# Kernel tuning notes

Hardware: AMD Instinct MI355X
Metric: run time of the kernel (lower is better)

Reference implementation:

```python
import jax, jax.numpy as jnp
import numpy as np

N, CS, CZ, H, C, PQ, PV, N0, N1 = 768, 384, 128, 12, 64, 4, 8, 192, 64
CZ4 = CZ // 4
INF, EPS = 1e5, 1e-8


def setup_inputs() -> dict:
    key = jax.random.key(0)
    ks = jax.random.split(key, 24)

    def w(k, i, o):
        return jax.random.normal(k, (i, o), jnp.float32) / np.float32(np.sqrt(i))

    s = jax.random.normal(ks[0], (N, CS), jnp.float32)
    z = jax.random.normal(ks[1], (N, N, CZ), jnp.float32)
    rot = jnp.linalg.qr(jax.random.normal(ks[2], (N, 3, 3), jnp.float32))[0]
    trans = jax.random.normal(ks[3], (N, 3), jnp.float32)
    mask = jnp.ones((N,), jnp.float32)
    is_atom = jax.random.bernoulli(ks[4], 0.5, (N,))
    return dict(
        s=s, z=z, rot=rot, trans=trans, mask=mask, is_atom=is_atom,
        wq=w(ks[5], CS, H * C), bq=jnp.zeros((H * C,), jnp.float32),
        wkv=w(ks[6], CS, 2 * H * C), bkv=jnp.zeros((2 * H * C,), jnp.float32),
        wqp=w(ks[7], CS, 3 * H * PQ), bqp=jnp.zeros((3 * H * PQ,), jnp.float32),
        wkvp=w(ks[8], CS, 3 * H * (PQ + PV)), bkvp=jnp.zeros((3 * H * (PQ + PV),), jnp.float32),
        wb=w(ks[9], CZ, H), bb=jnp.zeros((H,), jnp.float32),
        wdz=w(ks[10], CZ, CZ4), bdz=jnp.zeros((CZ4,), jnp.float32),
        head_weights=jnp.full((H,), 0.5413248, jnp.float32),  # softplus^-1(1), per ipa_point_weights_init_
        wout=w(ks[11], H * (C + 4 * PV + CZ4), CS), bout=jnp.zeros((CS,), jnp.float32),
        tfnq_ws=w(ks[12], N0, H * C), tfnq_wv=w(ks[13], N1, H * PQ),
        tfnkv_ws=w(ks[14], N0, 2 * H * C), tfnkv_wv=w(ks[15], N1, H * (PQ + PV)),
        tfno_ws=w(ks[16], H * (C + PV + CZ4), N0), tfno_wv=w(ks[17], H * PV, N1),
    )


def reference(s, z, rot, trans, mask, is_atom, wq, bq, wkv, bkv, wqp, bqp, wkvp, bkvp,
              wb, bb, wdz, bdz, head_weights, wout, bout,
              tfnq_ws, tfnq_wv, tfnkv_ws, tfnkv_wv, tfno_ws, tfno_wv):
    n = s.shape[0]

    def apply_rigid(pts):  # pts: [n, P, 3] -> R x + t
        return jnp.einsum('nij,npj->npi', rot, pts) + trans[:, None, :]

    # ---- residue (frame) path ----
    q_r = (s @ wq + bq).reshape(n, H, C)
    kv_r = (s @ wkv + bkv).reshape(n, H, 2 * C)
    k_r, v_r = kv_r[..., :C], kv_r[..., C:]
    # torch.split-in-3 then stack(dim=-1) layout: [n, 3, H*P] -> [n, H*P, 3]
    qp = (s @ wqp + bqp).reshape(n, 3, H * PQ).transpose(0, 2, 1)
    q_pts_r = apply_rigid(qp).reshape(n, H, PQ, 3)
    kvp = (s @ wkvp + bkvp).reshape(n, 3, H * (PQ + PV)).transpose(0, 2, 1)
    kv_pts_r = apply_rigid(kvp).reshape(n, H, PQ + PV, 3)
    k_pts_r, v_pts_r = kv_pts_r[..., :PQ, :], kv_pts_r[..., PQ:, :]

    # ---- atom (TFN-equivariant) path: irreps = N0 scalars + N1 vectors ----
    sc = s[:, :N0]
    vec = s[:, N0:N0 + 3 * N1].reshape(n, N1, 3)
    q_a = (sc @ tfnq_ws).reshape(n, H, C)
    q_pts_a = jnp.einsum('nix,io->nox', vec, tfnq_wv).reshape(n, H, PQ, 3) + trans[:, None, None, :]
    kv_a = (sc @ tfnkv_ws).reshape(n, H, 2 * C)
    k_a, v_a = kv_a[..., :C], kv_a[..., C:]
    kv_pts_a = jnp.einsum('nix,io->nox', vec, tfnkv_wv).reshape(n, H, PQ + PV, 3) + trans[:, None, None, :]
    k_pts_a, v_pts_a = kv_pts_a[..., :PQ, :], kv_pts_a[..., PQ:, :]

    m1 = is_atom[:, None, None]
    m2 = is_atom[:, None, None, None]
    q = jnp.where(m1, q_a, q_r)
    k = jnp.where(m1, k_a, k_r)
    v = jnp.where(m1, v_a, v_r)
    q_pts = jnp.where(m2, q_pts_a, q_pts_r)
    k_pts = jnp.where(m2, k_pts_a, k_pts_r)
    v_pts = jnp.where(m2, v_pts_a, v_pts_r)

    # ---- attention logits ----
    b = z @ wb + bb  # [n, n, H]
    a = jnp.einsum('nhc,mhc->hnm', q, k) * np.float32(np.sqrt(1.0 / (3 * C)))
    a = a + np.float32(np.sqrt(1.0 / 3)) * b.transpose(2, 0, 1)

    disp = q_pts[:, None] - k_pts[None]          # [n, n, H, PQ, 3]
    pt_att = jnp.sum(disp * disp, axis=-1)       # [n, n, H, PQ]
    hw = jax.nn.softplus(head_weights) * np.float32(np.sqrt(1.0 / (3 * (PQ * 9.0 / 2))))
    pt_att = -0.5 * jnp.sum(pt_att * hw[:, None], axis=-1)  # [n, n, H]
    a = a + pt_att.transpose(2, 0, 1)

    sq_mask = INF * (mask[:, None] * mask[None, :] - 1.0)
    a = jax.nn.softmax(a + sq_mask[None], axis=-1)  # [H, n, n]

    # ---- aggregation ----
    o = jnp.einsum('hnm,mhc->nhc', a, v).reshape(n, H * C)
    o_pt = jnp.einsum('hnm,mhpx->nhpx', a, v_pts)  # [n, H, PV, 3]
    o_pt = jnp.einsum('nji,nhpj->nhpi', rot, o_pt - trans[:, None, None, :])  # invert_apply
    o_pt_norm = jnp.sqrt(jnp.sum(o_pt * o_pt, axis=-1) + EPS).reshape(n, H * PV)
    o_pt = o_pt.reshape(n, H * PV, 3)
    pair_z = z @ wdz + bdz  # [n, n, CZ4]
    o_pair = jnp.einsum('hnm,nmz->nhz', a, pair_z).reshape(n, H * CZ4)

    # ---- residue output head ----
    res_feats = jnp.concatenate([o, o_pt[..., 0], o_pt[..., 1], o_pt[..., 2], o_pt_norm, o_pair], axis=-1)
    res_out = res_feats @ wout + bout  # [n, CS]

    # ---- atom output head (equivariant linear: scalars mix, vectors mix per-component) ----
    atom_sc = jnp.concatenate([o, o_pt_norm, o_pair], axis=-1) @ tfno_ws  # [n, N0]
    atom_vec = jnp.einsum('npx,po->nox', o_pt, tfno_wv).reshape(n, 3 * N1)
    atom_out = jnp.concatenate([atom_sc, atom_vec], axis=-1)  # [n, CS]

    return jnp.where(is_atom[:, None], atom_out, res_out)
```

## Files before the change

### kernel.cpp

```cpp
#include <hip/hip_runtime.h>
#include <hip/hip_bf16.h>

static constexpr int NN = 768;

typedef short v8bf __attribute__((ext_vector_type(8)));
typedef float v4f  __attribute__((ext_vector_type(4)));

__device__ __forceinline__ unsigned short f2bf(float f) {
  unsigned u = __float_as_uint(f);
  u += 0x7fffu + ((u >> 16) & 1u);
  return (unsigned short)(u >> 16);
}
__device__ __forceinline__ float bf2f(unsigned short s) {
  return __uint_as_float(((unsigned)s) << 16);
}

static constexpr size_t OFF_ISA    = 0;
static constexpr size_t OFF_WCT    = 1024;
static constexpr size_t OFF_BCAT   = 4096;
static constexpr size_t OFF_SBF    = 4160;
static constexpr size_t OFF_WQT    = 151616;
static constexpr size_t OFF_WKVT   = 299072;
static constexpr size_t OFF_WQPT   = 593984;
static constexpr size_t OFF_WKVPT  = 630848;
static constexpr size_t OFF_TFNQT  = 716864;
static constexpr size_t OFF_TFNKVT = 815168;
static constexpr size_t OFF_WOUTT  = 1011776;
static constexpr size_t OFF_TFNOT  = 1306688;
static constexpr size_t OFF_QR     = 1429568;
static constexpr size_t OFF_KVR    = 1724480;
static constexpr size_t OFF_QP     = 2314304;
static constexpr size_t OFF_KVP    = 2424896;
static constexpr size_t OFF_QA     = 2756672;
static constexpr size_t OFF_KVA    = 3051584;
static constexpr size_t OFF_QCAT   = 3641408;
static constexpr size_t OFF_KCAT   = 4083776;
static constexpr size_t OFF_RQ     = 4526144;
static constexpr size_t OFF_RK     = 4535360;
static constexpr size_t OFF_VCATT  = 4986944;
static constexpr size_t OFF_BB     = 5429312;
static constexpr size_t OFF_PZT    = 8968256;
static constexpr size_t OFF_ABF    = 18405440;
static constexpr size_t OFF_OPTRAW = 21944384;
static constexpr size_t OFF_RESF   = 22165568;
static constexpr size_t OFF_ATOMF  = 22755392;

__device__ void transpose_cv(const float* __restrict__ src, unsigned short* __restrict__ dst,
                             int K, int Kp, int N, int ky, int nx) {
  __shared__ float tl[32][33];
  const int k0 = ky * 32, n0 = nx * 32;
  const int tx = threadIdx.x & 31, ty = threadIdx.x >> 5;
  for (int it = 0; it < 4; ++it) {
    int r = ty + it * 8;
    float v = 0.f;
    if (k0 + r < K && n0 + tx < N) v = src[(long long)(k0 + r) * N + n0 + tx];
    tl[r][tx] = v;
  }
  __syncthreads();
  for (int it = 0; it < 4; ++it) {
    int r = ty + it * 8;
    if (n0 + r < N && k0 + tx < Kp)
      dst[(long long)(n0 + r) * Kp + k0 + tx] = f2bf(tl[tx][r]);
  }
}

__global__ __launch_bounds__(256) void prep0(
    float* wsf, const float* s, const float* wq, const float* wkv,
    const float* wqp, const float* wkvp, const float* tfnq_ws,
    const float* tfnkv_ws, const float* wout, const float* tfno_ws,
    const float* wb, const float* wdz, const float* bb, const float* bdz,
    const unsigned int* isa_raw)
{
  const int bx = blockIdx.x, t = threadIdx.x;
  if (bx < 288)       { int g = bx;        transpose_cv(wq,      (unsigned short*)(wsf+OFF_WQT),    384, 384, 768,  g/24, g%24); return; }
  else if (bx < 864)  { int g = bx-288;    transpose_cv(wkv,     (unsigned short*)(wsf+OFF_WKVT),   384, 384, 1536, g/48, g%48); return; }
  else if (bx < 924)  { int g = bx-864;    transpose_cv(wqp,     (unsigned short*)(wsf+OFF_WQPT),   384, 384, 144,  g/5,  g%5);  return; }
  else if (bx < 1092) { int g = bx-924;    transpose_cv(wkvp,    (unsigned short*)(wsf+OFF_WKVPT),  384, 384, 432,  g/14, g%14); return; }
  else if (bx < 1284) { int g = bx-1092;   transpose_cv(tfnq_ws, (unsigned short*)(wsf+OFF_TFNQT),  192, 256, 768,  g/24, g%24); return; }
  else if (bx < 1668) { int g = bx-1284;   transpose_cv(tfnkv_ws,(unsigned short*)(wsf+OFF_TFNKVT), 192, 256, 1536, g/48, g%48); return; }
  else if (bx < 2244) { int g = bx-1668;   transpose_cv(wout,    (unsigned short*)(wsf+OFF_WOUTT),  1536,1536,384,  g/12, g%12); return; }
  else if (bx < 2484) { int g = bx-2244;   transpose_cv(tfno_ws, (unsigned short*)(wsf+OFF_TFNOT),  1248,1280,192,  g/6,  g%6);  return; }
  else if (bx < 2772) {
    long long base = (long long)(bx - 2484) * 1024 + t * 4;
    float4 v = *(const float4*)(s + base);
    unsigned short tmp[4] = {f2bf(v.x), f2bf(v.y), f2bf(v.z), f2bf(v.w)};
    *(uint2*)((unsigned short*)(wsf + OFF_SBF) + base) = *(uint2*)tmp;
    return;
  } else if (bx < 2773) {
    __shared__ int notint, notfloat;
    int* ISA = (int*)(wsf + OFF_ISA);
    if (t == 0) { notint = 0; notfloat = 0; }
    __syncthreads();
    if (t < 192) {
      unsigned v = isa_raw[t];
      if (v > 1u) atomicOr(&notint, 1);
      if (v != 0u && v != 0x3F800000u) atomicOr(&notfloat, 1);
    }
    __syncthreads();
    const int mode = (!notint) ? 0 : ((!notfloat) ? 1 : 2);
    for (int n = t; n < NN; n += 256) {
      int val;
      if (mode == 2) val = (((const unsigned char*)isa_raw)[n] != 0);
      else           val = (isa_raw[n] != 0u);
      ISA[n] = val;
    }
    return;
  } else {
    const float rs3 = 0.57735026918962576f;
    unsigned short* WCT = (unsigned short*)(wsf + OFF_WCT);
    float* bcat = wsf + OFF_BCAT;
    int idx = (bx - 2773) * 256 + t;
    if (idx < 48 * 128) {
      int o = idx >> 7, k = idx & 127;
      float v = 0.f;
      if (o < 12) v = rs3 * wb[k * 12 + o];
      else if (o < 44) v = wdz[k * 32 + (o - 12)];
      WCT[o * 128 + k] = f2bf(v);
    }
    if (bx == 2773 && t < 48)
      bcat[t] = (t < 12) ? rs3 * bb[t] : (t < 44 ? bdz[t - 12] : 0.f);
  }
}

__device__ __forceinline__ void gemm16(
    char* lds, const unsigned short* __restrict__ A, int lda,
    const unsigned short* __restrict__ BT, int ldb, int KQ,
    const float* __restrict__ bias, int mode,
    float* Cf, unsigned short* Cb, int ldc, int Nc, int colb, int row0,
    const int* __restrict__ ISA, float* outp)
{
  v4f (*PS)[4][64] = (v4f (*)[4][64])lds;
  const int t = threadIdx.x, w = t >> 6, l = t & 63, l15 = l & 15, lg = l >> 4;
  const int rowA = row0 + l15;
  v4f acc[4] = {};
  const unsigned short* ap = A + (long long)rowA * lda + lg * 8;
  const int kend = (w + 1) * KQ;
  for (int k0 = w * KQ; k0 < kend; k0 += 32) {
    v8bf av = *(const v8bf*)(ap + k0);
#pragma unroll
    for (int cf = 0; cf < 4; ++cf) {
      v8bf bv = *(const v8bf*)(BT + (long long)(colb + cf * 16 + l15) * ldb + k0 + lg * 8);
      acc[cf] = __builtin_amdgcn_mfma_f32_16x16x32_bf16(av, bv, acc[cf], 0, 0, 0);
    }
  }
#pragma unroll
  for (int cf = 0; cf < 4; ++cf) PS[w][cf][l] = acc[cf];
  __syncthreads();
  const int cf = w;
  v4f sv = PS[0][cf][l] + PS[1][cf][l] + PS[2][cf][l] + PS[3][cf][l];
  const int c = colb + cf * 16 + l15;
  if (c < Nc) {
    float bvs = bias ? bias[c] : 0.f;
#pragma unroll
    for (int i = 0; i < 4; ++i) {
      int r = row0 + lg * 4 + i;
      float v = sv[i] + bvs;
      if (mode == 0)      Cf[(long long)r * ldc + c] = v;
      else if (mode == 1) Cb[(long long)r * ldc + c] = f2bf(v);
      else if (mode == 2) { if (!ISA[r]) outp[r * 384 + c] = v; }
      else                { if ( ISA[r]) outp[r * 384 + c] = v; }
    }
  }
}

__global__ __launch_bounds__(256) void mega1(
    float* wsf, const float* __restrict__ z,
    const float* bq, const float* bkv, const float* bqp, const float* bkvp)
{
  __shared__ __align__(16) char lds[23296];
  const int t = threadIdx.x;
  if (blockIdx.x < 4608) {
    float* Sout = (float*)lds;
    const unsigned short* WCT = (const unsigned short*)(wsf + OFF_WCT);
    const float* bcat = wsf + OFF_BCAT;
    unsigned short* Bb  = (unsigned short*)(wsf + OFF_BB);
    unsigned short* PZT = (unsigned short*)(wsf + OFF_PZT);
    const long long row0 = (long long)blockIdx.x * 128;
    const int w = t >> 6, l = t & 63, l15 = l & 15, lg = l >> 4;
    v8bf bvv[4][3];
#pragma unroll
    for (int ks = 0; ks < 4; ++ks)
#pragma unroll
      for (int cf = 0; cf < 3; ++cf)
        bvv[ks][cf] = *(const v8bf*)(WCT + (cf * 16 + l15) * 128 + ks * 32 + lg * 8);
    v4f acc[2][3] = {};
#pragma unroll
    for (int rf = 0; rf < 2; ++rf) {
      const float* zrow = z + (row0 + w * 32 + rf * 16 + l15) * 128 + lg * 8;
#pragma unroll
      for (int ks = 0; ks < 4; ++ks) {
        float4 a0 = *(const float4*)(zrow + ks * 32);
        float4 a1 = *(const float4*)(zrow + ks * 32 + 4);
        unsigned short tmp[8] = {f2bf(a0.x), f2bf(a0.y), f2bf(a0.z), f2bf(a0.w),
                                 f2bf(a1.x), f2bf(a1.y), f2bf(a1.z), f2bf(a1.w)};
        v8bf av = *(const v8bf*)tmp;
#pragma unroll
        for (int cf = 0; cf < 3; ++cf)
          acc[rf][cf] = __builtin_amdgcn_mfma_f32_16x16x32_bf16(av, bvv[ks][cf], acc[rf][cf], 0, 0, 0);
      }
    }
#pragma unroll
    for (int rf = 0; rf < 2; ++rf)
#pragma unroll
      for (int cf = 0; cf < 3; ++cf) {
        int o = cf * 16 + l15;
#pragma unroll
        for (int i = 0; i < 4; ++i) {
          int m = w * 32 + rf * 16 + lg * 4 + i;
          Sout[o * 132 + m] = acc[rf][cf][i];
        }
      }
    __syncthreads();
    const int n = blockIdx.x / 6;
    const int m0 = (blockIdx.x % 6) * 128;
    for (int idx = t; idx < 44 * 8; idx += 256) {
      int o = idx >> 3, seg = idx & 7;
      float bias = bcat[o];
      unsigned short tmp[16];
#pragma unroll
      for (int j = 0; j < 16; ++j) tmp[j] = f2bf(Sout[o * 132 + seg * 16 + j] + bias);
      unsigned short* gp;
      if (o < 12) gp = Bb + ((long long)o * 768 + n) * 768 + m0 + seg * 16;
      else        gp = PZT + ((long long)n * 32 + (o - 12)) * 768 + m0 + seg * 16;
      *(uint4*)gp = *(uint4*)tmp;
      *(uint4*)(gp + 8) = *(uint4*)(tmp + 8);
    }
    return;
  }
  const int g = blockIdx.x - 4608;
  const int bt = g / 82, xt = g % 82;
  const unsigned short* SBF = (const unsigned short*)(wsf + OFF_SBF);
  const unsigned short* BT; const float* bias; int ldb, KQ, mode, ldc, Nc, colb;
  float* Cf = nullptr; unsigned short* Cb = nullptr;
  if (xt < 12)      { BT=(const unsigned short*)(wsf+OFF_WQT);    bias=bq;     ldb=384; KQ=96; Cb=(unsigned short*)(wsf+OFF_QR);  ldc=768;  Nc=768;  colb=xt*64;      mode=1; }
  else if (xt < 36) { BT=(const unsigned short*)(wsf+OFF_WKVT);   bias=bkv;    ldb=384; KQ=96; Cb=(unsigned short*)(wsf+OFF_KVR); ldc=1536; Nc=1536; colb=(xt-12)*64; mode=1; }
  else if (xt < 39) { BT=(const unsigned short*)(wsf+OFF_WQPT);   bias=bqp;    ldb=384; KQ=96; Cf=wsf+OFF_QP;                     ldc=144;  Nc=144;  colb=(xt-36)*64; mode=0; }
  else if (xt < 46) { BT=(const unsigned short*)(wsf+OFF_WKVPT);  bias=bkvp;   ldb=384; KQ=96; Cf=wsf+OFF_KVP;                    ldc=432;  Nc=432;  colb=(xt-39)*64; mode=0; }
  else if (xt < 58) { BT=(const unsigned short*)(wsf+OFF_TFNQT);  bias=nullptr;ldb=256; KQ=64; Cb=(unsigned short*)(wsf+OFF_QA);  ldc=768;  Nc=768;  colb=(xt-46)*64; mode=1; }
  else              { BT=(const unsigned short*)(wsf+OFF_TFNKVT); bias=nullptr;ldb=256; KQ=64; Cb=(unsigned short*)(wsf+OFF_KVA); ldc=1536; Nc=1536; colb=(xt-58)*64; mode=1; }
  gemm16(lds, SBF, 384, BT, ldb, KQ, bias, mode, Cf, Cb, ldc, Nc, colb, bt * 16, nullptr, nullptr);
}

__global__ __launch_bounds__(256) void prep_qkv(
    float* wsf, const float* __restrict__ s,
    const float* __restrict__ rot, const float* __restrict__ trans,
    const float* __restrict__ head_w,
    const float* __restrict__ tfnq_wv, const float* __restrict__ tfnkv_wv)
{
  const int n = blockIdx.x, t = threadIdx.x;
  const int* ISA = (const int*)(wsf + OFF_ISA);
  const unsigned short* QRb  = (const unsigned short*)(wsf + OFF_QR);
  const unsigned short* KVRb = (const unsigned short*)(wsf + OFF_KVR);
  const unsigned short* QAb  = (const unsigned short*)(wsf + OFF_QA);
  const unsigned short* KVAb = (const unsigned short*)(wsf + OFF_KVA);
  const float* QP  = wsf + OFF_QP;
  const float* KVP = wsf + OFF_KVP;
  unsigned short* Qcat = (unsigned short*)(wsf + OFF_QCAT);
  unsigned short* Kcat = (unsigned short*)(wsf + OFF_KCAT);
  unsigned short* Vt   = (unsigned short*)(wsf + OFF_VCATT);
  float* rq = wsf + OFF_RQ;
  float* rk = wsf + OFF_RK;
  const bool isa = ISA[n] != 0;
  __shared__ float R[9], T[3], shw[12], sv[192];
  __shared__ float qs[768], ks[768], vs[768], qp[144], kp[144], vp[288];
  if (t < 9) R[t] = rot[n * 9 + t];
  if (t < 3) T[t] = trans[n * 3 + t];
  if (t >= 16 && t < 28)
    shw[t - 16] = log1pf(__expf(head_w[t - 16])) * 0.13608276348795434f;
  if (isa && t >= 32 && t < 224) sv[t - 32] = s[(size_t)n * 384 + 192 + (t - 32)];
  __syncthreads();
  for (int idx = t; idx < 768; idx += 256) {
    int h = idx >> 6, c = idx & 63;
    qs[idx] = bf2f(isa ? QAb[(long long)n * 768 + idx] : QRb[(long long)n * 768 + idx]);
    ks[idx] = bf2f(isa ? KVAb[(long long)n * 1536 + h * 128 + c] : KVRb[(long long)n * 1536 + h * 128 + c]);
    vs[idx] = bf2f(isa ? KVAb[(long long)n * 1536 + h * 128 + 64 + c] : KVRb[(long long)n * 1536 + h * 128 + 64 + c]);
  }
  if (isa) {
    for (int idx = t; idx < 144; idx += 256) {
      int hp = idx / 3, x = idx % 3;
      float a = 0.f;
      for (int i = 0; i < 64; ++i) a += sv[i * 3 + x] * tfnq_wv[i * 48 + hp];
      qp[idx] = a + T[x];
    }
    for (int idx = t; idx < 432; idx += 256) {
      int o = idx / 3, x = idx % 3;
      float a = 0.f;
      for (int i = 0; i < 64; ++i) a += sv[i * 3 + x] * tfnkv_wv[i * 144 + o];
      float v = a + T[x];
      int h = o / 12, pp = o % 12;
      if (pp < 4) kp[(h * 4 + pp) * 3 + x] = v;
      else        vp[(h * 8 + (pp - 4)) * 3 + x] = v;
    }
  } else {
    for (int idx = t; idx < 144; idx += 256) {
      int hp = idx / 3, i = idx % 3;
      qp[idx] = R[i * 3 + 0] * QP[(long long)n * 144 + 0 + hp] +
                R[i * 3 + 1] * QP[(long long)n * 144 + 48 + hp] +
                R[i * 3 + 2] * QP[(long long)n * 144 + 96 + hp] + T[i];
    }
    for (int idx = t; idx < 432; idx += 256) {
      int hp = idx / 3, i = idx % 3;
      float v = R[i * 3 + 0] * KVP[(long long)n * 432 + 0 + hp] +
                R[i * 3 + 1] * KVP[(long long)n * 432 + 144 + hp] +
                R[i * 3 + 2] * KVP[(long long)n * 432 + 288 + hp] + T[i];
      int h = hp / 12, pp = hp % 12;
      if (pp < 4) kp[(h * 4 + pp) * 3 + i] = v;
      else        vp[(h * 8 + (pp - 4)) * 3 + i] = v;
    }
  }
  __syncthreads();
  const float sq = 0.07216878364870322f;
  for (int idx = t; idx < 1152; idx += 256) {
    int h = idx / 96, c = idx % 96;
    float qv = (c < 64) ? sq * qs[h * 64 + c] : ((c < 76) ? shw[h] * qp[h * 12 + (c - 64)] : 0.f);
    float kv = (c < 64) ? ks[h * 64 + c]      : ((c < 76) ? kp[h * 12 + (c - 64)] : 0.f);
    float vv = (c < 64) ? vs[h * 64 + c]      : ((c < 88) ? vp[h * 24 + (c - 64)] : 0.f);
    long long base = ((long long)n * 12 + h) * 96 + c;
    Qcat[base] = f2bf(qv);
    Kcat[base] = f2bf(kv);
    Vt[((long long)h * 96 + c) * 768 + n] = f2bf(vv);
  }
  if (t < 24) {
    int h = t >> 1, which = t & 1;
    const float* p = which ? kp : qp;
    float s2 = 0.f;
#pragma unroll
    for (int d = 0; d < 12; ++d) { float x = p[h * 12 + d]; s2 += x * x; }
    float val = 0.5f * shw[h] * s2;
    if (which) rk[h * 768 + n] = val;
    else       rq[h * 768 + n] = val;
  }
}

__global__ __launch_bounds__(256) void mega2(float* wsf, const float* __restrict__ mask) {
  __shared__ __align__(16) char lds[26112];
  const int t = threadIdx.x;
  const unsigned short* Qcat = (const unsigned short*)(wsf + OFF_QCAT);
  const unsigned short* Kcat = (const unsigned short*)(wsf + OFF_KCAT);
  const unsigned short* Bb   = (const unsigned short*)(wsf + OFF_BB);
  const unsigned short* VcatT= (const unsigned short*)(wsf + OFF_VCATT);
  const float* rq = wsf + OFF_RQ;
  const float* rk = wsf + OFF_RK;
  unsigned short* Abf   = (unsigned short*)(wsf + OFF_ABF);
  unsigned short* RESF  = (unsigned short*)(wsf + OFF_RESF);
  unsigned short* ATOMF = (unsigned short*)(wsf + OFF_ATOMF);
  float* OPTRAW = wsf + OFF_OPTRAW;
  const int h = blockIdx.x / 48, r0 = (blockIdx.x % 48) * 16;
  const int w = t >> 6, l = t & 63, l15 = l & 15, lg = l >> 4;
  unsigned short* SW = (unsigned short*)lds + w * 3200;
  float* redm = (float*)(lds + 25600);
  float* reds = (float*)(lds + 25856);
  const int nrow = r0 + l15;
  v8bf aq[3];
#pragma unroll
  for (int ks = 0; ks < 3; ++ks)
    aq[ks] = *(const v8bf*)(Qcat + ((long long)nrow * 12 + h) * 96 + ks * 32 + lg * 8);
  v4f acc[12] = {};
#pragma unroll
  for (int cf = 0; cf < 12; ++cf) {
    int m = w * 192 + cf * 16 + l15;
    const unsigned short* kb = Kcat + ((long long)m * 12 + h) * 96 + lg * 8;
#pragma unroll
    for (int ks = 0; ks < 3; ++ks) {
      v8bf bv = *(const v8bf*)(kb + ks * 32);
      acc[cf] = __builtin_amdgcn_mfma_f32_16x16x32_bf16(aq[ks], bv, acc[cf], 0, 0, 0);
    }
  }
#pragma unroll
  for (int it = 0; it < 6; ++it) {
    int chunk = it * 64 + l;
    int row = chunk / 24, cc = (chunk % 24) * 8;
    *(uint4*)(SW + row * 200 + cc) =
        *(const uint4*)(Bb + ((long long)(h * 768 + r0 + row)) * 768 + w * 192 + cc);
  }
  __syncthreads();
  float rkm[12], mkm[12];
#pragma unroll
  for (int cf = 0; cf < 12; ++cf) {
    int m = w * 192 + cf * 16 + l15;
    rkm[cf] = rk[h * 768 + m];
    mkm[cf] = mask[m];
  }
  float rqn[4], mkn[4], mymax[4];
#pragma unroll
  for (int i = 0; i < 4; ++i) {
    int gn = r0 + lg * 4 + i;
    rqn[i] = rq[h * 768 + gn];
    mkn[i] = mask[gn];
    mymax[i] = -3.0e38f;
  }
#pragma unroll
  for (int cf = 0; cf < 12; ++cf)
#pragma unroll
    for (int i = 0; i < 4; ++i) {
      float v = acc[cf][i] + bf2f(SW[(lg * 4 + i) * 200 + cf * 16 + l15])
              - rqn[i] - rkm[cf] + 100000.0f * (mkn[i] * mkm[cf] - 1.0f);
      acc[cf][i] = v;
      mymax[i] = fmaxf(mymax[i], v);
    }
#pragma unroll
  for (int off = 1; off < 16; off <<= 1)
#pragma unroll
    for (int i = 0; i < 4; ++i) mymax[i] = fmaxf(mymax[i], __shfl_xor(mymax[i], off, 64));
  if (l15 == 0) {
#pragma unroll
    for (int i = 0; i < 4; ++i) redm[w * 16 + lg * 4 + i] = mymax[i];
  }
  __syncthreads();
  float mx[4], mysum[4];
#pragma unroll
  for (int i = 0; i < 4; ++i) {
    int rl = lg * 4 + i;
    mx[i] = fmaxf(fmaxf(redm[rl], redm[16 + rl]), fmaxf(redm[32 + rl], redm[48 + rl]));
    mysum[i] = 0.f;
  }
#pragma unroll
  for (int cf = 0; cf < 12; ++cf)
#pragma unroll
    for (int i = 0; i < 4; ++i) {
      float e = __expf(acc[cf][i] - mx[i]);
      acc[cf][i] = e;
      mysum[i] += e;
    }
#pragma unroll
  for (int off = 1; off < 16; off <<= 1)
#pragma unroll
    for (int i = 0; i < 4; ++i) mysum[i] += __shfl_xor(mysum[i], off, 64);
  if (l15 == 0) {
#pragma unroll
    for (int i = 0; i < 4; ++i) reds[w * 16 + lg * 4 + i] = mysum[i];
  }
  __syncthreads();
  float inv[4];
#pragma unroll
  for (int i = 0; i < 4; ++i) {
    int rl = lg * 4 + i;
    inv[i] = 1.0f / (reds[rl] + reds[16 + rl] + reds[32 + rl] + reds[48 + rl]);
  }
#pragma unroll
  for (int cf = 0; cf < 12; ++cf)
#pragma unroll
    for (int i = 0; i < 4; ++i)
      SW[(lg * 4 + i) * 200 + cf * 16 + l15] = f2bf(acc[cf][i] * inv[i]);
  __syncthreads();
#pragma unroll
  for (int it = 0; it < 6; ++it) {
    int chunk = it * 64 + l;
    int row = chunk / 24, cc = (chunk % 24) * 8;
    *(uint4*)(Abf + ((long long)(h * 768 + r0 + row)) * 768 + w * 192 + cc) =
        *(const uint4*)(SW + row * 200 + cc);
  }
  const unsigned short* vbase = VcatT + (long long)h * 96 * 768 + w * 192 + lg * 8;
  v4f acc2[6] = {};
  for (int kk = 0; kk < 192; kk += 32) {
    v8bf av = *(const v8bf*)(SW + l15 * 200 + kk + lg * 8);
#pragma unroll
    for (int cf = 0; cf < 6; ++cf) {
      v8bf bv = *(const v8bf*)(vbase + (long long)(cf * 16 + l15) * 768 + kk);
      acc2[cf] = __builtin_amdgcn_mfma_f32_16x16x32_bf16(av, bv, acc2[cf], 0, 0, 0);
    }
  }
  __syncthreads();
  v4f (*PS)[64] = (v4f (*)[64])lds;
#pragma unroll
  for (int cf = 0; cf < 6; ++cf) PS[w * 6 + cf][l] = acc2[cf];
  __syncthreads();
  for (int cf = w; cf < 6; cf += 4) {
    v4f sv = PS[cf][l] + PS[6 + cf][l] + PS[12 + cf][l] + PS[18 + cf][l];
    int c = cf * 16 + l15;
    int rb = r0 + lg * 4;
#pragma unroll
    for (int i = 0; i < 4; ++i) {
      int n = rb + i;
      float v = sv[i];
      if (c < 64) {
        unsigned short b = f2bf(v);
        RESF[(long long)n * 1536 + h * 64 + c] = b;
        ATOMF[(long long)n * 1280 + h * 64 + c] = b;
      } else if (c < 88) {
        OPTRAW[(long long)n * 288 + h * 24 + (c - 64)] = v;
      }
    }
  }
}

__global__ __launch_bounds__(256) void mega3(
    float* wsf, const float* __restrict__ rot, const float* __restrict__ trans,
    const float* __restrict__ tfno_wv, float* __restrict__ out)
{
  const int t = threadIdx.x;
  unsigned short* RESF  = (unsigned short*)(wsf + OFF_RESF);
  unsigned short* ATOMF = (unsigned short*)(wsf + OFF_ATOMF);
  if (blockIdx.x < 768) {
    __shared__ __align__(16) v4f PS[8][64];
    const unsigned short* Abf = (const unsigned short*)(wsf + OFF_ABF);
    const unsigned short* PZT = (const unsigned short*)(wsf + OFF_PZT);
    const int w = t >> 6, l = t & 63, l15 = l & 15, lg = l >> 4;
    const int n = blockIdx.x;
    const int hh = (l15 < 12) ? l15 : 0;
    const unsigned short* arow = Abf + ((long long)hh * 768 + n) * 768 + lg * 8;
    const unsigned short* pz = PZT + (long long)n * 32 * 768 + lg * 8;
    v4f acc[2] = {};
    for (int k0 = w * 192; k0 < w * 192 + 192; k0 += 32) {
      v8bf av = *(const v8bf*)(arow + k0);
#pragma unroll
      for (int cf = 0; cf < 2; ++cf) {
        v8bf bv = *(const v8bf*)(pz + (long long)(cf * 16 + l15) * 768 + k0);
        acc[cf] = __builtin_amdgcn_mfma_f32_16x16x32_bf16(av, bv, acc[cf], 0, 0, 0);
      }
    }
    PS[w * 2 + 0][l] = acc[0];
    PS[w * 2 + 1][l] = acc[1];
    __syncthreads();
    if (t < 128) {
      int cf = t >> 6, ll = t & 63;
      v4f sv = PS[cf][ll] + PS[2 + cf][ll] + PS[4 + cf][ll] + PS[6 + cf][ll];
      int zc = cf * 16 + (ll & 15);
#pragma unroll
      for (int i = 0; i < 4; ++i) {
        int hd = (ll >> 4) * 4 + i;
        if (hd < 12) {
          unsigned short b = f2bf(sv[i]);
          RESF[(long long)n * 1536 + 1152 + hd * 32 + zc] = b;
          ATOMF[(long long)n * 1280 + 864 + hd * 32 + zc] = b;
        }
      }
    }
    return;
  }
  {
    const int n = blockIdx.x - 768;
    const float* OPTRAW = wsf + OFF_OPTRAW;
    const int* ISA = (const int*)(wsf + OFF_ISA);
    const bool isa = ISA[n] != 0;
    __shared__ float R[9], T[3], opt2[96][3], norml[96];
    if (t < 9) R[t] = rot[(size_t)n * 9 + t];
    if (t < 3) T[t] = trans[(size_t)n * 3 + t];
    __syncthreads();
    for (int idx = t; idx < 288; idx += 256) {
      int hp = idx / 3, i = idx % 3;
      float x = OPTRAW[(size_t)n * 288 + hp * 3 + 0] - T[0];
      float y = OPTRAW[(size_t)n * 288 + hp * 3 + 1] - T[1];
      float z = OPTRAW[(size_t)n * 288 + hp * 3 + 2] - T[2];
      opt2[hp][i] = R[0 + i] * x + R[3 + i] * y + R[6 + i] * z;
    }
    __syncthreads();
    if (t < 96)
      norml[t] = sqrtf(opt2[t][0] * opt2[t][0] + opt2[t][1] * opt2[t][1] +
                       opt2[t][2] * opt2[t][2] + 1e-8f);
    __syncthreads();
    const long long rb = (long long)n * 1536;
    const long long ab = (long long)n * 1280;
    for (int idx = t; idx < 288; idx += 256) {
      int x = idx / 96, hp = idx % 96;
      RESF[rb + 768 + idx] = f2bf(opt2[hp][x]);
    }
    for (int idx = t; idx < 96; idx += 256) {
      unsigned short b = f2bf(norml[idx]);
      RESF[rb + 1056 + idx] = b;
      ATOMF[ab + 768 + idx] = b;
    }
    if (isa) {
      for (int idx = t; idx < 192; idx += 256) {
        int o = idx / 3, x = idx % 3;
        float a = 0.f;
        for (int p = 0; p < 96; ++p) a += opt2[p][x] * tfno_wv[p * 64 + o];
        out[(size_t)n * 384 + 192 + idx] = a;
      }
    }
  }
}

__global__ __launch_bounds__(256) void outg(float* wsf, const float* __restrict__ bout,
                                            float* __restrict__ out) {
  __shared__ __align__(16) char lds[16384];
  const int g = blockIdx.x;
  const int bt = g / 9, xt = g % 9;
  const int* ISA = (const int*)(wsf + OFF_ISA);
  if (xt < 6)
    gemm16(lds, (const unsigned short*)(wsf + OFF_RESF), 1536,
           (const unsigned short*)(wsf + OFF_WOUTT), 1536, 384, bout, 2,
           nullptr, nullptr, 0, 384, xt * 64, bt * 16, ISA, out);
  else
    gemm16(lds, (const unsigned short*)(wsf + OFF_ATOMF), 1280,
           (const unsigned short*)(wsf + OFF_TFNOT), 1280, 320, nullptr, 3,
           nullptr, nullptr, 0, 192, (xt - 6) * 64, bt * 16, ISA, out);
}

extern "C" void kernel_launch(void* const* d_in, const int* in_sizes, int n_in,
                              void* d_out, int out_size, void* d_ws, size_t ws_size,
                              hipStream_t stream) {
  (void)in_sizes; (void)n_in; (void)out_size; (void)ws_size;
  const float* s      = (const float*)d_in[0];
  const float* z      = (const float*)d_in[1];
  const float* rot    = (const float*)d_in[2];
  const float* trans  = (const float*)d_in[3];
  const float* mask   = (const float*)d_in[4];
  const float* wq     = (const float*)d_in[6];
  const float* bq     = (const float*)d_in[7];
  const float* wkv    = (const float*)d_in[8];
  const float* bkv    = (const float*)d_in[9];
  const float* wqp    = (const float*)d_in[10];
  const float* bqp    = (const float*)d_in[11];
  const float* wkvp   = (const float*)d_in[12];
  const float* bkvp   = (const float*)d_in[13];
  const float* wb     = (const float*)d_in[14];
  const float* bb     = (const float*)d_in[15];
  const float* wdz    = (const float*)d_in[16];
  const float* bdz    = (const float*)d_in[17];
  const float* head_w = (const float*)d_in[18];
  const float* wout   = (const float*)d_in[19];
  const float* bout   = (const float*)d_in[20];
  const float* tfnq_ws  = (const float*)d_in[21];
  const float* tfnq_wv  = (const float*)d_in[22];
  const float* tfnkv_ws = (const float*)d_in[23];
  const float* tfnkv_wv = (const float*)d_in[24];
  const float* tfno_ws  = (const float*)d_in[25];
  const float* tfno_wv  = (const float*)d_in[26];

  float* wsf = (float*)d_ws;

  prep0<<<2797, 256, 0, stream>>>(wsf, s, wq, wkv, wqp, wkvp, tfnq_ws, tfnkv_ws,
                                  wout, tfno_ws, wb, wdz, bb, bdz,
                                  (const unsigned int*)d_in[5]);
  mega1<<<8544, 256, 0, stream>>>(wsf, z, bq, bkv, bqp, bkvp);
  prep_qkv<<<768, 256, 0, stream>>>(wsf, s, rot, trans, head_w, tfnq_wv, tfnkv_wv);
  mega2<<<576, 256, 0, stream>>>(wsf, mask);
  mega3<<<1536, 256, 0, stream>>>(wsf, rot, trans, tfno_wv, (float*)d_out);
  outg<<<432, 256, 0, stream>>>(wsf, bout, (float*)d_out);
}
```

Before: 186.1 us.

## Split z-projection pass across two kernels to overlap with weight prep and GEMMs

The large z projection pass (4608 blocks) moves out of a single kernel and is split into two halves. The first half runs alongside the weight transposes and the s conversion, and the second half runs alongside the projection GEMMs. The small WCT/bias/is_atom setup moves into a tiny leading kernel because the z pass depends on it. The goal is to hide the prep work and the GEMM tail behind the memory-bound z streaming, at the cost of one extra kernel launch; an unroll pragma is also added in mega2.

After: 200.2 us. +7.6%, slower.

```diff
diff --git a/kernel.cpp b/kernel.cpp
--- a/kernel.cpp
+++ b/kernel.cpp
@@ -45,9 +45,50 @@
 static constexpr size_t OFF_RESF   = 22165568;
 static constexpr size_t OFF_ATOMF  = 22755392;
 
-__device__ void transpose_cv(const float* __restrict__ src, unsigned short* __restrict__ dst,
+__global__ __launch_bounds__(256) void tiny0(
+    float* wsf, const float* __restrict__ wb, const float* __restrict__ wdz,
+    const float* __restrict__ bb, const float* __restrict__ bdz,
+    const unsigned int* __restrict__ isa_raw)
+{
+  const int t = threadIdx.x;
+  if (blockIdx.x == 0) {
+    const float rs3 = 0.57735026918962576f;
+    unsigned short* WCT = (unsigned short*)(wsf + OFF_WCT);
+    float* bcat = wsf + OFF_BCAT;
+    for (int idx = t; idx < 48 * 128; idx += 256) {
+      int o = idx >> 7, k = idx & 127;
+      float v = 0.f;
+      if (o < 12) v = rs3 * wb[k * 12 + o];
+      else if (o < 44) v = wdz[k * 32 + (o - 12)];
+      WCT[o * 128 + k] = f2bf(v);
+    }
+    if (t < 48)
+      bcat[t] = (t < 12) ? rs3 * bb[t] : (t < 44 ? bdz[t - 12] : 0.f);
+  } else {
+    __shared__ int notint, notfloat;
+    int* ISA = (int*)wsf;
+    if (t == 0) { notint = 0; notfloat = 0; }
+    __syncthreads();
+    if (t < 192) {
+      unsigned v = isa_raw[t];
+      if (v > 1u) atomicOr(&notint, 1);
+      if (v != 0u && v != 0x3F800000u) atomicOr(&notfloat, 1);
+    }
+    __syncthreads();
+    const int mode = (!notint) ? 0 : ((!notfloat) ? 1 : 2);
+    for (int n = t; n < NN; n += 256) {
+      int val;
+      if (mode == 2) val = (((const unsigned char*)isa_raw)[n] != 0);
+      else           val = (isa_raw[n] != 0u);
+      ISA[n] = val;
+    }
+  }
+}
+
+__device__ void transpose_cv(char* ldsbuf, const float* __restrict__ src,
+                             unsigned short* __restrict__ dst,
                              int K, int Kp, int N, int ky, int nx) {
-  __shared__ float tl[32][33];
+  float (*tl)[33] = (float (*)[33])ldsbuf;
   const int k0 = ky * 32, n0 = nx * 32;
   const int tx = threadIdx.x & 31, ty = threadIdx.x >> 5;
   for (int it = 0; it < 4; ++it) {
@@ -61,64 +102,6 @@
     int r = ty + it * 8;
     if (n0 + r < N && k0 + tx < Kp)
       dst[(long long)(n0 + r) * Kp + k0 + tx] = f2bf(tl[tx][r]);
-  }
-}
-
-__global__ __launch_bounds__(256) void prep0(
-    float* wsf, const float* s, const float* wq, const float* wkv,
-    const float* wqp, const float* wkvp, const float* tfnq_ws,
-    const float* tfnkv_ws, const float* wout, const float* tfno_ws,
-    const float* wb, const float* wdz, const float* bb, const float* bdz,
-    const unsigned int* isa_raw)
-{
-  const int bx = blockIdx.x, t = threadIdx.x;
-  if (bx < 288)       { int g = bx;        transpose_cv(wq,      (unsigned short*)(wsf+OFF_WQT),    384, 384, 768,  g/24, g%24); return; }
-  else if (bx < 864)  { int g = bx-288;    transpose_cv(wkv,     (unsigned short*)(wsf+OFF_WKVT),   384, 384, 1536, g/48, g%48); return; }
-  else if (bx < 924)  { int g = bx-864;    transpose_cv(wqp,     (unsigned short*)(wsf+OFF_WQPT),   384, 384, 144,  g/5,  g%5);  return; }
-  else if (bx < 1092) { int g = bx-924;    transpose_cv(wkvp,    (unsigned short*)(wsf+OFF_WKVPT),  384, 384, 432,  g/14, g%14); return; }
-  else if (bx < 1284) { int g = bx-1092;   transpose_cv(tfnq_ws, (unsigned short*)(wsf+OFF_TFNQT),  192, 256, 768,  g/24, g%24); return; }
-  else if (bx < 1668) { int g = bx-1284;   transpose_cv(tfnkv_ws,(unsigned short*)(wsf+OFF_TFNKVT), 192, 256, 1536, g/48, g%48); return; }
-  else if (bx < 2244) { int g = bx-1668;   transpose_cv(wout,    (unsigned short*)(wsf+OFF_WOUTT),  1536,1536,384,  g/12, g%12); return; }
-  else if (bx < 2484) { int g = bx-2244;   transpose_cv(tfno_ws, (unsigned short*)(wsf+OFF_TFNOT),  1248,1280,192,  g/6,  g%6);  return; }
-  else if (bx < 2772) {
-    long long base = (long long)(bx - 2484) * 1024 + t * 4;
-    float4 v = *(const float4*)(s + base);
-    unsigned short tmp[4] = {f2bf(v.x), f2bf(v.y), f2bf(v.z), f2bf(v.w)};
-    *(uint2*)((unsigned short*)(wsf + OFF_SBF) + base) = *(uint2*)tmp;
-    return;
-  } else if (bx < 2773) {
-    __shared__ int notint, notfloat;
-    int* ISA = (int*)(wsf + OFF_ISA);
-    if (t == 0) { notint = 0; notfloat = 0; }
-    __syncthreads();
-    if (t < 192) {
-      unsigned v = isa_raw[t];
-      if (v > 1u) atomicOr(&notint, 1);
-      if (v != 0u && v != 0x3F800000u) atomicOr(&notfloat, 1);
-    }
-    __syncthreads();
-    const int mode = (!notint) ? 0 : ((!notfloat) ? 1 : 2);
-    for (int n = t; n < NN; n += 256) {
-      int val;
-      if (mode == 2) val = (((const unsigned char*)isa_raw)[n] != 0);
-      else           val = (isa_raw[n] != 0u);
-      ISA[n] = val;
-    }
-    return;
-  } else {
-    const float rs3 = 0.57735026918962576f;
-    unsigned short* WCT = (unsigned short*)(wsf + OFF_WCT);
-    float* bcat = wsf + OFF_BCAT;
-    int idx = (bx - 2773) * 256 + t;
-    if (idx < 48 * 128) {
-      int o = idx >> 7, k = idx & 127;
-      float v = 0.f;
-      if (o < 12) v = rs3 * wb[k * 12 + o];
-      else if (o < 44) v = wdz[k * 32 + (o - 12)];
-      WCT[o * 128 + k] = f2bf(v);
-    }
-    if (bx == 2773 && t < 48)
-      bcat[t] = (t < 12) ? rs3 * bb[t] : (t < 44 ? bdz[t - 12] : 0.f);
   }
 }
 
@@ -163,71 +146,96 @@
   }
 }
 
-__global__ __launch_bounds__(256) void mega1(
+__device__ void zpass_body(char* lds, float* wsf, const float* __restrict__ z, int bx) {
+  const int t = threadIdx.x;
+  float* Sout = (float*)lds;
+  const unsigned short* WCT = (const unsigned short*)(wsf + OFF_WCT);
+  const float* bcat = wsf + OFF_BCAT;
+  unsigned short* Bb  = (unsigned short*)(wsf + OFF_BB);
+  unsigned short* PZT = (unsigned short*)(wsf + OFF_PZT);
+  const long long row0 = (long long)bx * 128;
+  const int w = t >> 6, l = t & 63, l15 = l & 15, lg = l >> 4;
+  v8bf bvv[4][3];
+#pragma unroll
+  for (int ks = 0; ks < 4; ++ks)
+#pragma unroll
+    for (int cf = 0; cf < 3; ++cf)
+      bvv[ks][cf] = *(const v8bf*)(WCT + (cf * 16 + l15) * 128 + ks * 32 + lg * 8);
+  v4f acc[2][3] = {};
+#pragma unroll
+  for (int rf = 0; rf < 2; ++rf) {
+    const float* zrow = z + (row0 + w * 32 + rf * 16 + l15) * 128 + lg * 8;
+#pragma unroll
+    for (int ks = 0; ks < 4; ++ks) {
+      float4 a0 = *(const float4*)(zrow + ks * 32);
+      float4 a1 = *(const float4*)(zrow + ks * 32 + 4);
+      unsigned short tmp[8] = {f2bf(a0.x), f2bf(a0.y), f2bf(a0.z), f2bf(a0.w),
+                               f2bf(a1.x), f2bf(a1.y), f2bf(a1.z), f2bf(a1.w)};
+      v8bf av = *(const v8bf*)tmp;
+#pragma unroll
+      for (int cf = 0; cf < 3; ++cf)
+        acc[rf][cf] = __builtin_amdgcn_mfma_f32_16x16x32_bf16(av, bvv[ks][cf], acc[rf][cf], 0, 0, 0);
+    }
+  }
+#pragma unroll
+  for (int rf = 0; rf < 2; ++rf)
+#pragma unroll
+    for (int cf = 0; cf < 3; ++cf) {
+      int o = cf * 16 + l15;
+#pragma unroll
+      for (int i = 0; i < 4; ++i) {
+        int m = w * 32 + rf * 16 + lg * 4 + i;
+        Sout[o * 132 + m] = acc[rf][cf][i];
+      }
+    }
+  __syncthreads();
+  const int n = bx / 6;
+  const int m0 = (bx % 6) * 128;
+  for (int idx = t; idx < 44 * 8; idx += 256) {
+    int o = idx >> 3, seg = idx & 7;
+    float bias = bcat[o];
+    unsigned short tmp[16];
+#pragma unroll
+    for (int j = 0; j < 16; ++j) tmp[j] = f2bf(Sout[o * 132 + seg * 16 + j] + bias);
+    unsigned short* gp;
+    if (o < 12) gp = Bb + ((long long)o * 768 + n) * 768 + m0 + seg * 16;
+    else        gp = PZT + ((long long)n * 32 + (o - 12)) * 768 + m0 + seg * 16;
+    *(uint4*)gp = *(uint4*)tmp;
+    *(uint4*)(gp + 8) = *(uint4*)(tmp + 8);
+  }
+}
+
+__global__ __launch_bounds__(256) void zmix1(
+    float* wsf, const float* __restrict__ z, const float* s,
+    const float* wq, const float* wkv, const float* wqp, const float* wkvp,
+    const float* tfnq_ws, const float* tfnkv_ws, const float* wout, const float* tfno_ws)
+{
+  __shared__ __align__(16) char lds[23296];
+  if (blockIdx.x < 2304) { zpass_body(lds, wsf, z, blockIdx.x); return; }
+  const int vb = blockIdx.x - 2304;
+  if (vb < 288)       { transpose_cv(lds, wq,       (unsigned short*)(wsf+OFF_WQT),    384, 384, 768,  vb/24,        vb%24); }
+  else if (vb < 864)  { int g = vb-288;  transpose_cv(lds, wkv,      (unsigned short*)(wsf+OFF_WKVT),   384, 384, 1536, g/48, g%48); }
+  else if (vb < 924)  { int g = vb-864;  transpose_cv(lds, wqp,      (unsigned short*)(wsf+OFF_WQPT),   384, 384, 144,  g/5,  g%5);  }
+  else if (vb < 1092) { int g = vb-924;  transpose_cv(lds, wkvp,     (unsigned short*)(wsf+OFF_WKVPT),  384, 384, 432,  g/14, g%14); }
+  else if (vb < 1284) { int g = vb-1092; transpose_cv(lds, tfnq_ws,  (unsigned short*)(wsf+OFF_TFNQT),  192, 256, 768,  g/24, g%24); }
+  else if (vb < 1668) { int g = vb-1284; transpose_cv(lds, tfnkv_ws, (unsigned short*)(wsf+OFF_TFNKVT), 192, 256, 1536, g/48, g%48); }
+  else if (vb < 2244) { int g = vb-1668; transpose_cv(lds, wout,     (unsigned short*)(wsf+OFF_WOUTT),  1536,1536,384,  g/12, g%12); }
+  else if (vb < 2484) { int g = vb-2244; transpose_cv(lds, tfno_ws,  (unsigned short*)(wsf+OFF_TFNOT),  1248,1280,192,  g/6,  g%6);  }
+  else {
+    long long base = (long long)(vb - 2484) * 1024 + threadIdx.x * 4;
+    float4 v = *(const float4*)(s + base);
+    unsigned short tmp[4] = {f2bf(v.x), f2bf(v.y), f2bf(v.z), f2bf(v.w)};
+    *(uint2*)((unsigned short*)(wsf + OFF_SBF) + base) = *(uint2*)tmp;
+  }
+}
+
+__global__ __launch_bounds__(256) void zmix2(
     float* wsf, const float* __restrict__ z,
     const float* bq, const float* bkv, const float* bqp, const float* bkvp)
 {
   __shared__ __align__(16) char lds[23296];
-  const int t = threadIdx.x;
-  if (blockIdx.x < 4608) {
-    float* Sout = (float*)lds;
-    const unsigned short* WCT = (const unsigned short*)(wsf + OFF_WCT);
-    const float* bcat = wsf + OFF_BCAT;
-    unsigned short* Bb  = (unsigned short*)(wsf + OFF_BB);
-    unsigned short* PZT = (unsigned short*)(wsf + OFF_PZT);
-    const long long row0 = (long long)blockIdx.x * 128;
-    const int w = t >> 6, l = t & 63, l15 = l & 15, lg = l >> 4;
-    v8bf bvv[4][3];
-#pragma unroll
-    for (int ks = 0; ks < 4; ++ks)
-#pragma unroll
-      for (int cf = 0; cf < 3; ++cf)
-        bvv[ks][cf] = *(const v8bf*)(WCT + (cf * 16 + l15) * 128 + ks * 32 + lg * 8);
-    v4f acc[2][3] = {};
-#pragma unroll
-    for (int rf = 0; rf < 2; ++rf) {
-      const float* zrow = z + (row0 + w * 32 + rf * 16 + l15) * 128 + lg * 8;
-#pragma unroll
-      for (int ks = 0; ks < 4; ++ks) {
-        float4 a0 = *(const float4*)(zrow + ks * 32);
-        float4 a1 = *(const float4*)(zrow + ks * 32 + 4);
-        unsigned short tmp[8] = {f2bf(a0.x), f2bf(a0.y), f2bf(a0.z), f2bf(a0.w),
-                                 f2bf(a1.x), f2bf(a1.y), f2bf(a1.z), f2bf(a1.w)};
-        v8bf av = *(const v8bf*)tmp;
-#pragma unroll
-        for (int cf = 0; cf < 3; ++cf)
-          acc[rf][cf] = __builtin_amdgcn_mfma_f32_16x16x32_bf16(av, bvv[ks][cf], acc[rf][cf], 0, 0, 0);
-      }
-    }
-#pragma unroll
-    for (int rf = 0; rf < 2; ++rf)
-#pragma unroll
-      for (int cf = 0; cf < 3; ++cf) {
-        int o = cf * 16 + l15;
-#pragma unroll
-        for (int i = 0; i < 4; ++i) {
-          int m = w * 32 + rf * 16 + lg * 4 + i;
-          Sout[o * 132 + m] = acc[rf][cf][i];
-        }
-      }
-    __syncthreads();
-    const int n = blockIdx.x / 6;
-    const int m0 = (blockIdx.x % 6) * 128;
-    for (int idx = t; idx < 44 * 8; idx += 256) {
-      int o = idx >> 3, seg = idx & 7;
-      float bias = bcat[o];
-      unsigned short tmp[16];
-#pragma unroll
-      for (int j = 0; j < 16; ++j) tmp[j] = f2bf(Sout[o * 132 + seg * 16 + j] + bias);
-      unsigned short* gp;
-      if (o < 12) gp = Bb + ((long long)o * 768 + n) * 768 + m0 + seg * 16;
-      else        gp = PZT + ((long long)n * 32 + (o - 12)) * 768 + m0 + seg * 16;
-      *(uint4*)gp = *(uint4*)tmp;
-      *(uint4*)(gp + 8) = *(uint4*)(tmp + 8);
-    }
-    return;
-  }
-  const int g = blockIdx.x - 4608;
+  if (blockIdx.x < 2304) { zpass_body(lds, wsf, z, blockIdx.x + 2304); return; }
+  const int g = blockIdx.x - 2304;
   const int bt = g / 82, xt = g % 82;
   const unsigned short* SBF = (const unsigned short*)(wsf + OFF_SBF);
   const unsigned short* BT; const float* bias; int ldb, KQ, mode, ldc, Nc, colb;
@@ -248,7 +256,7 @@
     const float* __restrict__ tfnq_wv, const float* __restrict__ tfnkv_wv)
 {
   const int n = blockIdx.x, t = threadIdx.x;
-  const int* ISA = (const int*)(wsf + OFF_ISA);
+  const int* ISA = (const int*)wsf;
   const unsigned short* QRb  = (const unsigned short*)(wsf + OFF_QR);
   const unsigned short* KVRb = (const unsigned short*)(wsf + OFF_KVR);
   const unsigned short* QAb  = (const unsigned short*)(wsf + OFF_QA);
@@ -452,6 +460,7 @@
   }
   const unsigned short* vbase = VcatT + (long long)h * 96 * 768 + w * 192 + lg * 8;
   v4f acc2[6] = {};
+#pragma unroll
   for (int kk = 0; kk < 192; kk += 32) {
     v8bf av = *(const v8bf*)(SW + l15 * 200 + kk + lg * 8);
 #pragma unroll
@@ -531,7 +540,7 @@
   {
     const int n = blockIdx.x - 768;
     const float* OPTRAW = wsf + OFF_OPTRAW;
-    const int* ISA = (const int*)(wsf + OFF_ISA);
+    const int* ISA = (const int*)wsf;
     const bool isa = ISA[n] != 0;
     __shared__ float R[9], T[3], opt2[96][3], norml[96];
     if (t < 9) R[t] = rot[(size_t)n * 9 + t];
@@ -576,7 +585,7 @@
   __shared__ __align__(16) char lds[16384];
   const int g = blockIdx.x;
   const int bt = g / 9, xt = g % 9;
-  const int* ISA = (const int*)(wsf + OFF_ISA);
+  const int* ISA = (const int*)wsf;
   if (xt < 6)
     gemm16(lds, (const unsigned short*)(wsf + OFF_RESF), 1536,
            (const unsigned short*)(wsf + OFF_WOUTT), 1536, 384, bout, 2,
@@ -620,10 +629,10 @@
 
   float* wsf = (float*)d_ws;
 
-  prep0<<<2797, 256, 0, stream>>>(wsf, s, wq, wkv, wqp, wkvp, tfnq_ws, tfnkv_ws,
-                                  wout, tfno_ws, wb, wdz, bb, bdz,
-                                  (const unsigned int*)d_in[5]);
-  mega1<<<8544, 256, 0, stream>>>(wsf, z, bq, bkv, bqp, bkvp);
+  tiny0<<<2, 256, 0, stream>>>(wsf, wb, wdz, bb, bdz, (const unsigned int*)d_in[5]);
+  zmix1<<<5076, 256, 0, stream>>>(wsf, z, s, wq, wkv, wqp, wkvp,
+                                  tfnq_ws, tfnkv_ws, wout, tfno_ws);
+  zmix2<<<6240, 256, 0, stream>>>(wsf, z, bq, bkv, bqp, bkvp);
   prep_qkv<<<768, 256, 0, stream>>>(wsf, s, rot, trans, head_w, tfnq_wv, tfnkv_wv);
   mega2<<<576, 256, 0, stream>>>(wsf, mask);
   mega3<<<1536, 256, 0, stream>>>(wsf, rot, trans, tfno_wv, (float*)d_out);
```

## Split attention kernel into 8-row blocks to double grid size

Applied to the files above, without the earlier changes.

The attention/softmax kernel now handles 8 query rows per block instead of 16, doubling the grid from 576 to 1152 blocks to improve occupancy across CUs. The MFMA tiles still compute 16 rows, so half the lanes do masked, wasted work, and K/V loads are repeated across twice as many blocks. The ISA pointer is also rewritten as the workspace base, which is equivalent because its offset is 0. An unroll pragma is added to the aggregation loop.

Result: slower. 217.0 us (+16.6%).

```diff
diff --git a/kernel.cpp b/kernel.cpp
--- a/kernel.cpp
+++ b/kernel.cpp
@@ -88,7 +88,7 @@
     return;
   } else if (bx < 2773) {
     __shared__ int notint, notfloat;
-    int* ISA = (int*)(wsf + OFF_ISA);
+    int* ISA = (int*)wsf;
     if (t == 0) { notint = 0; notfloat = 0; }
     __syncthreads();
     if (t < 192) {
@@ -248,7 +248,7 @@
     const float* __restrict__ tfnq_wv, const float* __restrict__ tfnkv_wv)
 {
   const int n = blockIdx.x, t = threadIdx.x;
-  const int* ISA = (const int*)(wsf + OFF_ISA);
+  const int* ISA = (const int*)wsf;
   const unsigned short* QRb  = (const unsigned short*)(wsf + OFF_QR);
   const unsigned short* KVRb = (const unsigned short*)(wsf + OFF_KVR);
   const unsigned short* QAb  = (const unsigned short*)(wsf + OFF_QA);
@@ -345,16 +345,18 @@
   unsigned short* RESF  = (unsigned short*)(wsf + OFF_RESF);
   unsigned short* ATOMF = (unsigned short*)(wsf + OFF_ATOMF);
   float* OPTRAW = wsf + OFF_OPTRAW;
-  const int h = blockIdx.x / 48, r0 = (blockIdx.x % 48) * 16;
+  const int h = blockIdx.x / 96, r0 = (blockIdx.x % 96) * 8;
   const int w = t >> 6, l = t & 63, l15 = l & 15, lg = l >> 4;
   unsigned short* SW = (unsigned short*)lds + w * 3200;
   float* redm = (float*)(lds + 25600);
-  float* reds = (float*)(lds + 25856);
+  float* reds = (float*)(lds + 25728);
+  const bool vrow = (lg < 2);
   const int nrow = r0 + l15;
+  const int nr = (nrow < 768) ? nrow : 767;
   v8bf aq[3];
 #pragma unroll
   for (int ks = 0; ks < 3; ++ks)
-    aq[ks] = *(const v8bf*)(Qcat + ((long long)nrow * 12 + h) * 96 + ks * 32 + lg * 8);
+    aq[ks] = *(const v8bf*)(Qcat + ((long long)nr * 12 + h) * 96 + ks * 32 + lg * 8);
   v4f acc[12] = {};
 #pragma unroll
   for (int cf = 0; cf < 12; ++cf) {
@@ -367,7 +369,7 @@
     }
   }
 #pragma unroll
-  for (int it = 0; it < 6; ++it) {
+  for (int it = 0; it < 3; ++it) {
     int chunk = it * 64 + l;
     int row = chunk / 24, cc = (chunk % 24) * 8;
     *(uint4*)(SW + row * 200 + cc) =
@@ -384,7 +386,8 @@
   float rqn[4], mkn[4], mymax[4];
 #pragma unroll
   for (int i = 0; i < 4; ++i) {
-    int gn = r0 + lg * 4 + i;
+    int rl = lg * 4 + i;
+    int gn = vrow ? (r0 + rl) : 0;
     rqn[i] = rq[h * 768 + gn];
     mkn[i] = mask[gn];
     mymax[i] = -3.0e38f;
@@ -393,8 +396,10 @@
   for (int cf = 0; cf < 12; ++cf)
 #pragma unroll
     for (int i = 0; i < 4; ++i) {
-      float v = acc[cf][i] + bf2f(SW[(lg * 4 + i) * 200 + cf * 16 + l15])
-              - rqn[i] - rkm[cf] + 100000.0f * (mkn[i] * mkm[cf] - 1.0f);
+      int rl = lg * 4 + i;
+      float bbv = vrow ? bf2f(SW[rl * 200 + cf * 16 + l15]) : 0.f;
+      float v = acc[cf][i] + bbv - rqn[i] - rkm[cf]
+              + 100000.0f * (mkn[i] * mkm[cf] - 1.0f);
       acc[cf][i] = v;
       mymax[i] = fmaxf(mymax[i], v);
     }
@@ -402,16 +407,17 @@
   for (int off = 1; off < 16; off <<= 1)
 #pragma unroll
     for (int i = 0; i < 4; ++i) mymax[i] = fmaxf(mymax[i], __shfl_xor(mymax[i], off, 64));
-  if (l15 == 0) {
-#pragma unroll
-    for (int i = 0; i < 4; ++i) redm[w * 16 + lg * 4 + i] = mymax[i];
+  if (l15 == 0 && vrow) {
+#pragma unroll
+    for (int i = 0; i < 4; ++i) redm[w * 8 + lg * 4 + i] = mymax[i];
   }
   __syncthreads();
   float mx[4], mysum[4];
 #pragma unroll
   for (int i = 0; i < 4; ++i) {
     int rl = lg * 4 + i;
-    mx[i] = fmaxf(fmaxf(redm[rl], redm[16 + rl]), fmaxf(redm[32 + rl], redm[48 + rl]));
+    mx[i] = vrow ? fmaxf(fmaxf(redm[rl], redm[8 + rl]), fmaxf(redm[16 + rl], redm[24 + rl]))
+                 : 3.0e38f;
     mysum[i] = 0.f;
   }
 #pragma unroll
@@ -426,25 +432,27 @@
   for (int off = 1; off < 16; off <<= 1)
 #pragma unroll
     for (int i = 0; i < 4; ++i) mysum[i] += __shfl_xor(mysum[i], off, 64);
-  if (l15 == 0) {
-#pragma unroll
-    for (int i = 0; i < 4; ++i) reds[w * 16 + lg * 4 + i] = mysum[i];
+  if (l15 == 0 && vrow) {
+#pragma unroll
+    for (int i = 0; i < 4; ++i) reds[w * 8 + lg * 4 + i] = mysum[i];
   }
   __syncthreads();
   float inv[4];
 #pragma unroll
   for (int i = 0; i < 4; ++i) {
     int rl = lg * 4 + i;
-    inv[i] = 1.0f / (reds[rl] + reds[16 + rl] + reds[32 + rl] + reds[48 + rl]);
+    inv[i] = vrow ? 1.0f / (reds[rl] + reds[8 + rl] + reds[16 + rl] + reds[24 + rl]) : 0.f;
   }
 #pragma unroll
   for (int cf = 0; cf < 12; ++cf)
 #pragma unroll
-    for (int i = 0; i < 4; ++i)
-      SW[(lg * 4 + i) * 200 + cf * 16 + l15] = f2bf(acc[cf][i] * inv[i]);
-  __syncthreads();
-#pragma unroll
-  for (int it = 0; it < 6; ++it) {
+    for (int i = 0; i < 4; ++i) {
+      int rl = lg * 4 + i;
+      SW[rl * 200 + cf * 16 + l15] = vrow ? f2bf(acc[cf][i] * inv[i]) : 0;
+    }
+  __syncthreads();
+#pragma unroll
+  for (int it = 0; it < 3; ++it) {
     int chunk = it * 64 + l;
     int row = chunk / 24, cc = (chunk % 24) * 8;
     *(uint4*)(Abf + ((long long)(h * 768 + r0 + row)) * 768 + w * 192 + cc) =
@@ -452,6 +460,7 @@
   }
   const unsigned short* vbase = VcatT + (long long)h * 96 * 768 + w * 192 + lg * 8;
   v4f acc2[6] = {};
+#pragma unroll
   for (int kk = 0; kk < 192; kk += 32) {
     v8bf av = *(const v8bf*)(SW + l15 * 200 + kk + lg * 8);
 #pragma unroll
@@ -468,17 +477,19 @@
   for (int cf = w; cf < 6; cf += 4) {
     v4f sv = PS[cf][l] + PS[6 + cf][l] + PS[12 + cf][l] + PS[18 + cf][l];
     int c = cf * 16 + l15;
-    int rb = r0 + lg * 4;
-#pragma unroll
-    for (int i = 0; i < 4; ++i) {
-      int n = rb + i;
-      float v = sv[i];
-      if (c < 64) {
-        unsigned short b = f2bf(v);
-        RESF[(long long)n * 1536 + h * 64 + c] = b;
-        ATOMF[(long long)n * 1280 + h * 64 + c] = b;
-      } else if (c < 88) {
-        OPTRAW[(long long)n * 288 + h * 24 + (c - 64)] = v;
+    if (vrow) {
+      int rb = r0 + lg * 4;
+#pragma unroll
+      for (int i = 0; i < 4; ++i) {
+        int n = rb + i;
+        float v = sv[i];
+        if (c < 64) {
+          unsigned short b = f2bf(v);
+          RESF[(long long)n * 1536 + h * 64 + c] = b;
+          ATOMF[(long long)n * 1280 + h * 64 + c] = b;
+        } else if (c < 88) {
+          OPTRAW[(long long)n * 288 + h * 24 + (c - 64)] = v;
+        }
       }
     }
   }
@@ -531,7 +542,7 @@
   {
     const int n = blockIdx.x - 768;
     const float* OPTRAW = wsf + OFF_OPTRAW;
-    const int* ISA = (const int*)(wsf + OFF_ISA);
+    const int* ISA = (const int*)wsf;
     const bool isa = ISA[n] != 0;
     __shared__ float R[9], T[3], opt2[96][3], norml[96];
     if (t < 9) R[t] = rot[(size_t)n * 9 + t];
@@ -576,7 +587,7 @@
   __shared__ __align__(16) char lds[16384];
   const int g = blockIdx.x;
   const int bt = g / 9, xt = g % 9;
-  const int* ISA = (const int*)(wsf + OFF_ISA);
+  const int* ISA = (const int*)wsf;
   if (xt < 6)
     gemm16(lds, (const unsigned short*)(wsf + OFF_RESF), 1536,
            (const unsigned short*)(wsf + OFF_WOUTT), 1536, 384, bout, 2,
@@ -625,7 +636,7 @@
                                   (const unsigned int*)d_in[5]);
   mega1<<<8544, 256, 0, stream>>>(wsf, z, bq, bkv, bqp, bkvp);
   prep_qkv<<<768, 256, 0, stream>>>(wsf, s, rot, trans, head_w, tfnq_wv, tfnkv_wv);
-  mega2<<<576, 256, 0, stream>>>(wsf, mask);
+  mega2<<<1152, 256, 0, stream>>>(wsf, mask);
   mega3<<<1536, 256, 0, stream>>>(wsf, rot, trans, tfno_wv, (float*)d_out);
   outg<<<432, 256, 0, stream>>>(wsf, bout, (float*)d_out);
 }
```
